# Kernel tuning notes

Hardware: AMD Instinct MI355X
Metric: run time of the kernel (lower is better)

Reference implementation:

```python
import jax, jax.numpy as jnp
import numpy as np

N_HEADS = 16
LOCAL_WINDOW = 256
GLOBAL_WINDOW = 1024


def _block_mha(x, in_proj_w, in_proj_b, out_proj_w, out_proj_b, window, n_heads):
    """Non-overlapping sliding-window MHA, matching torch nn.MultiheadAttention math.

    x: [B, S, D]; windows are independent -> fold them into the batch dim and do
    one batched attention (block-diagonal attention over the sequence).
    """
    B, S, D = x.shape
    nw = S // window
    hd = D // n_heads
    xw = x.reshape(B * nw, window, D)
    # combined QKV projection: in_proj_w is [3D, D], torch applies x @ W^T + b
    qkv = xw @ in_proj_w.T + in_proj_b  # [B*nw, W, 3D]
    q, k, v = jnp.split(qkv, 3, axis=-1)
    q = q.reshape(B * nw, window, n_heads, hd)
    k = k.reshape(B * nw, window, n_heads, hd)
    v = v.reshape(B * nw, window, n_heads, hd)
    scale = 1.0 / np.sqrt(hd).astype(np.float32)
    scores = jnp.einsum('bqhd,bkhd->bhqk', q, k) * scale
    attn = jax.nn.softmax(scores, axis=-1)
    out = jnp.einsum('bhqk,bkhd->bqhd', attn, v).reshape(B * nw, window, D)
    out = out @ out_proj_w.T + out_proj_b
    return out.reshape(B, S, D)


def setup_inputs() -> dict:
    key = jax.random.key(0)
    ks = jax.random.split(key, 8)
    B, S, D = 2, 4096, 1024
    w_scale = 1.0 / np.sqrt(D).astype(np.float32)
    return {
        'lqs': jax.random.normal(ks[0], (B, S, D), dtype=jnp.float32),
        'gqs': jax.random.normal(ks[1], (B, S, D), dtype=jnp.float32),
        'in_proj_w_l': jax.random.normal(ks[2], (3 * D, D), dtype=jnp.float32) * w_scale,
        'in_proj_b_l': jnp.zeros((3 * D,), dtype=jnp.float32),
        'out_proj_w_l': jax.random.normal(ks[3], (D, D), dtype=jnp.float32) * w_scale,
        'out_proj_b_l': jnp.zeros((D,), dtype=jnp.float32),
        'in_proj_w_g': jax.random.normal(ks[4], (3 * D, D), dtype=jnp.float32) * w_scale,
        'in_proj_b_g': jnp.zeros((3 * D,), dtype=jnp.float32),
        'out_proj_w_g': jax.random.normal(ks[5], (D, D), dtype=jnp.float32) * w_scale,
        'out_proj_b_g': jnp.zeros((D,), dtype=jnp.float32),
    }


def reference(lqs, gqs, in_proj_w_l, in_proj_b_l, out_proj_w_l, out_proj_b_l,
              in_proj_w_g, in_proj_b_g, out_proj_w_g, out_proj_b_g):
    local_out = _block_mha(lqs, in_proj_w_l, in_proj_b_l, out_proj_w_l, out_proj_b_l,
                           LOCAL_WINDOW, N_HEADS)
    global_out = _block_mha(gqs, in_proj_w_g, in_proj_b_g, out_proj_w_g, out_proj_b_g,
                            GLOBAL_WINDOW, N_HEADS)
    return (local_out, global_out)
```

## Files before the change

kernel.cpp:

```cpp
#include <hip/hip_runtime.h>
#include <stdint.h>

typedef __attribute__((ext_vector_type(8))) __bf16 bf16x8;
typedef __attribute__((ext_vector_type(4))) float f32x4;

__device__ __forceinline__ void async_ld16(const void* g, void* l) {
  __builtin_amdgcn_global_load_lds(
      (const __attribute__((address_space(1))) unsigned int*)g,
      (__attribute__((address_space(3))) unsigned int*)l, 16, 0, 0);
}

__device__ __forceinline__ unsigned short f2bf(float x) {
  union { float f; unsigned int u; } v; v.f = x;
  unsigned int r = v.u + 0x7FFFu + ((v.u >> 16) & 1u);
  return (unsigned short)(r >> 16);
}

__device__ __forceinline__ float exp2_fast(float x) {
  return __builtin_amdgcn_exp2f(x);
}

__device__ __forceinline__ unsigned int pack_bf2(float a, float b) {
  unsigned int ua = __builtin_bit_cast(unsigned int, a) + 0x8000u;
  unsigned int ub = __builtin_bit_cast(unsigned int, b) + 0x8000u;
  return __builtin_amdgcn_perm(ub, ua, 0x07060302u);
}

__global__ void cvt3(const float* __restrict__ x, unsigned short* __restrict__ xd,
                     const float* __restrict__ w1, unsigned short* __restrict__ w1d,
                     const float* __restrict__ w2, unsigned short* __restrict__ w2d) {
  int i = blockIdx.x * 256 + threadIdx.x;
  const float* s; unsigned short* d; int off;
  if (i < 2097152)      { s = x;  d = xd;  off = i; }
  else if (i < 2883584) { s = w1; d = w1d; off = i - 2097152; }
  else                  { s = w2; d = w2d; off = i - 2883584; }
  float4 v = ((const float4*)s)[off];
  ushort4 o;
  o.x = f2bf(v.x); o.y = f2bf(v.y); o.z = f2bf(v.z); o.w = f2bf(v.w);
  ((ushort4*)d)[off] = o;
}

__global__ __launch_bounds__(512, 2)
void gemm_bt(const unsigned short* __restrict__ A0, const unsigned short* __restrict__ A1,
             const unsigned short* __restrict__ B0, const unsigned short* __restrict__ B1,
             const float* __restrict__ bias0, const float* __restrict__ bias1,
             void* __restrict__ out0, void* __restrict__ out1,
             int N, int K, int f32out, int qlim, float qs) {
  __shared__ unsigned short As[2][2][256 * 32];
  __shared__ unsigned short Bs[2][2][256 * 32];
  int br = blockIdx.z;
  const unsigned short* A = br ? A1 : A0;
  const unsigned short* B = br ? B1 : B0;
  const float* bias = br ? bias1 : bias0;
  void* outp = br ? out1 : out0;

  int gx = gridDim.x, gy = gridDim.y;
  int nwg = gx * gy;
  int flat = blockIdx.y * gx + blockIdx.x;
  int cpx = nwg >> 3;
  int swb = (flat & 7) * cpx + (flat >> 3);
  int bxi = swb % gx, byi = swb / gx;

  int tid = threadIdx.x;
  int wave = tid >> 6, lane = tid & 63;
  int quad = lane >> 4, l16 = lane & 15;
  int wm = (wave >> 2) * 128;
  int wn = (wave & 3) * 64;
  size_t bm = (size_t)byi * 256, bn = (size_t)bxi * 256;

  f32x4 acc[8][4];
  f32x4 zero = {0.f, 0.f, 0.f, 0.f};
#pragma unroll
  for (int i = 0; i < 8; i++)
#pragma unroll
    for (int j = 0; j < 4; j++) acc[i][j] = zero;

  int swc = (quad ^ ((l16 >> 1) & 3)) * 16;
  const char* ArdB = (const char*)As + (wm + l16) * 64 + swc;
  const char* BrdB = (const char*)Bs + (wn + l16) * 64 + swc;

  int row0 = tid >> 2, c0 = (tid & 3) ^ ((row0 >> 1) & 3);
  int row1 = row0 + 128, c1 = (tid & 3) ^ ((row1 >> 1) & 3);
  const char* Ag0 = (const char*)(A + (bm + row0) * (size_t)K) + c0 * 16;
  const char* Ag1 = (const char*)(A + (bm + row1) * (size_t)K) + c1 * 16;
  const char* Bg0 = (const char*)(B + (bn + row0) * (size_t)K) + c0 * 16;
  const char* Bg1 = (const char*)(B + (bn + row1) * (size_t)K) + c1 * 16;
  char* ldsA = (char*)As + tid * 16;
  char* ldsB = (char*)Bs + tid * 16;

#define STAGE_A(po_, kh_, koff_) do {                    \
    char* d_ = ldsA + (po_) + (kh_) * 16384;             \
    async_ld16(Ag0 + (koff_), d_);                       \
    async_ld16(Ag1 + (koff_), d_ + 8192); } while (0)
#define STAGE_B(po_, kh_, koff_) do {                    \
    char* d_ = ldsB + (po_) + (kh_) * 16384;             \
    async_ld16(Bg0 + (koff_), d_);                       \
    async_ld16(Bg1 + (koff_), d_ + 8192); } while (0)
#define LDA_F(po_, kh_, mi_) (*(const bf16x8*)(ArdB + (po_) + (kh_) * 16384 + (mi_) * 1024))
#define LDB_F(po_, kh_, ni_) (*(const bf16x8*)(BrdB + (po_) + (kh_) * 16384 + (ni_) * 1024))
#define BAR() do { __builtin_amdgcn_s_barrier(); asm volatile("" ::: "memory"); } while (0)
#define MFMAQ(mb_) do {                                                                              \
    acc[(mb_)+0][0] = __builtin_amdgcn_mfma_f32_16x16x32_bf16(b0, a0, acc[(mb_)+0][0], 0, 0, 0);     \
    acc[(mb_)+1][0] = __builtin_amdgcn_mfma_f32_16x16x32_bf16(b0, a1, acc[(mb_)+1][0], 0, 0, 0);     \
    acc[(mb_)+2][0] = __builtin_amdgcn_mfma_f32_16x16x32_bf16(b0, a2, acc[(mb_)+2][0], 0, 0, 0);     \
    acc[(mb_)+3][0] = __builtin_amdgcn_mfma_f32_16x16x32_bf16(b0, a3, acc[(mb_)+3][0], 0, 0, 0);     \
    acc[(mb_)+0][1] = __builtin_amdgcn_mfma_f32_16x16x32_bf16(b1, a0, acc[(mb_)+0][1], 0, 0, 0);     \
    acc[(mb_)+1][1] = __builtin_amdgcn_mfma_f32_16x16x32_bf16(b1, a1, acc[(mb_)+1][1], 0, 0, 0);     \
    acc[(mb_)+2][1] = __builtin_amdgcn_mfma_f32_16x16x32_bf16(b1, a2, acc[(mb_)+2][1], 0, 0, 0);     \
    acc[(mb_)+3][1] = __builtin_amdgcn_mfma_f32_16x16x32_bf16(b1, a3, acc[(mb_)+3][1], 0, 0, 0);     \
    acc[(mb_)+0][2] = __builtin_amdgcn_mfma_f32_16x16x32_bf16(b2, a0, acc[(mb_)+0][2], 0, 0, 0);     \
    acc[(mb_)+1][2] = __builtin_amdgcn_mfma_f32_16x16x32_bf16(b2, a1, acc[(mb_)+1][2], 0, 0, 0);     \
    acc[(mb_)+2][2] = __builtin_amdgcn_mfma_f32_16x16x32_bf16(b2, a2, acc[(mb_)+2][2], 0, 0, 0);     \
    acc[(mb_)+3][2] = __builtin_amdgcn_mfma_f32_16x16x32_bf16(b2, a3, acc[(mb_)+3][2], 0, 0, 0);     \
    acc[(mb_)+0][3] = __builtin_amdgcn_mfma_f32_16x16x32_bf16(b3, a0, acc[(mb_)+0][3], 0, 0, 0);     \
    acc[(mb_)+1][3] = __builtin_amdgcn_mfma_f32_16x16x32_bf16(b3, a1, acc[(mb_)+1][3], 0, 0, 0);     \
    acc[(mb_)+2][3] = __builtin_amdgcn_mfma_f32_16x16x32_bf16(b3, a2, acc[(mb_)+2][3], 0, 0, 0);     \
    acc[(mb_)+3][3] = __builtin_amdgcn_mfma_f32_16x16x32_bf16(b3, a3, acc[(mb_)+3][3], 0, 0, 0);     \
  } while (0)

  const int NT = K >> 6;

  STAGE_A(0, 0, 0);       STAGE_B(0, 0, 0);
  STAGE_A(0, 1, 64);      STAGE_B(0, 1, 64);
  STAGE_A(32768, 0, 128); STAGE_B(32768, 0, 128);
  asm volatile("s_waitcnt vmcnt(4)" ::: "memory");
  BAR();

  for (int j = 0; j < NT; ++j) {
    int po = (j & 1) * 32768;
    int qo = po ^ 32768;
    int t1 = (j + 1 < NT) ? j + 1 : NT - 1;
    int t2 = (j + 2 < NT) ? j + 2 : NT - 1;
    int ko1 = t1 * 128 + 64;
    int ko2 = t2 * 128;
    bf16x8 a0, a1, a2, a3, b0, b1, b2, b3;

    b0 = LDB_F(po, 0, 0); b1 = LDB_F(po, 0, 1); b2 = LDB_F(po, 0, 2); b3 = LDB_F(po, 0, 3);
    a0 = LDA_F(po, 0, 0); a1 = LDA_F(po, 0, 1); a2 = LDA_F(po, 0, 2); a3 = LDA_F(po, 0, 3);
    STAGE_A(qo, 1, ko1);
    __builtin_amdgcn_s_setprio(1); MFMAQ(0); __builtin_amdgcn_s_setprio(0);
    BAR();
    a0 = LDA_F(po, 0, 4); a1 = LDA_F(po, 0, 5); a2 = LDA_F(po, 0, 6); a3 = LDA_F(po, 0, 7);
    STAGE_B(qo, 1, ko1);
    __builtin_amdgcn_s_setprio(1); MFMAQ(4); __builtin_amdgcn_s_setprio(0);
    asm volatile("s_waitcnt vmcnt(8)" ::: "memory");
    BAR();
    b0 = LDB_F(po, 1, 0); b1 = LDB_F(po, 1, 1); b2 = LDB_F(po, 1, 2); b3 = LDB_F(po, 1, 3);
    a0 = LDA_F(po, 1, 0); a1 = LDA_F(po, 1, 1); a2 = LDA_F(po, 1, 2); a3 = LDA_F(po, 1, 3);
    STAGE_A(po, 0, ko2);
    __builtin_amdgcn_s_setprio(1); MFMAQ(0); __builtin_amdgcn_s_setprio(0);
    BAR();
    a0 = LDA_F(po, 1, 4); a1 = LDA_F(po, 1, 5); a2 = LDA_F(po, 1, 6); a3 = LDA_F(po, 1, 7);
    STAGE_B(po, 0, ko2);
    __builtin_amdgcn_s_setprio(1); MFMAQ(4); __builtin_amdgcn_s_setprio(0);
    asm volatile("s_waitcnt vmcnt(8)" ::: "memory");
    BAR();
  }

#undef STAGE_A
#undef STAGE_B
#undef LDA_F
#undef LDB_F
#undef BAR
#undef MFMAQ

#pragma unroll
  for (int mi = 0; mi < 8; mi++) {
    size_t rowg = bm + wm + mi * 16 + l16;
#pragma unroll
    for (int ni = 0; ni < 4; ni++) {
      size_t col = bn + wn + ni * 16 + quad * 4;
      float s = ((int)col < qlim) ? qs : 1.0f;
      float4 bv = *(const float4*)&bias[col];
      f32x4 a = acc[mi][ni];
      if (f32out) {
        float4 o = {(a[0] + bv.x) * s, (a[1] + bv.y) * s,
                    (a[2] + bv.z) * s, (a[3] + bv.w) * s};
        *(float4*)&((float*)outp)[rowg * N + col] = o;
      } else {
        ushort4 o;
        o.x = f2bf((a[0] + bv.x) * s); o.y = f2bf((a[1] + bv.y) * s);
        o.z = f2bf((a[2] + bv.z) * s); o.w = f2bf((a[3] + bv.w) * s);
        *(ushort4*)&((unsigned short*)outp)[rowg * N + col] = o;
      }
    }
  }
}

__device__ __forceinline__ int kperm(int p) {
  return (p & 0xC3) | ((p & 0x0C) << 2) | ((p & 0x30) >> 2);
}
__global__ void transpose_v(const unsigned short* __restrict__ q0, unsigned short* __restrict__ v0, int W0,
                            const unsigned short* __restrict__ q1, unsigned short* __restrict__ v1, int W1,
                            int zsplit) {
  __shared__ unsigned short tile[64][33];
  int z = blockIdx.z;
  const unsigned short* qkv; unsigned short* vt; int W, wb, yy;
  if (z < zsplit) { qkv = q0; vt = v0; W = W0; wb = z; yy = blockIdx.y; }
  else { qkv = q1; vt = v1; W = W1; int t = z - zsplit; wb = t >> 2; yy = blockIdx.y + 4 * (t & 3); }
  int c0 = blockIdx.x * 32, w0 = yy * 64;
  const unsigned short* src = qkv + (size_t)wb * W * 3072 + 2048;
  for (int i = threadIdx.y; i < 64; i += 8)
    tile[i][threadIdx.x] = src[(size_t)(w0 + i) * 3072 + c0 + threadIdx.x];
  __syncthreads();
  unsigned short* dst = vt + (size_t)wb * 1024 * W;
  for (int i = threadIdx.y; i < 32; i += 8) {
    int p0 = threadIdx.x, p1 = threadIdx.x + 32;
    dst[(size_t)(c0 + i) * W + w0 + p0] = tile[kperm(p0)][i];
    dst[(size_t)(c0 + i) * W + w0 + p1] = tile[kperm(p1)][i];
  }
}

__global__ __launch_bounds__(256)
void attn_fused(const unsigned short* __restrict__ qkv0, const unsigned short* __restrict__ vt0,
                unsigned short* __restrict__ ao0, int W0, int nb0,
                const unsigned short* __restrict__ qkv1, const unsigned short* __restrict__ vt1,
                unsigned short* __restrict__ ao1, int W1) {
  __shared__ unsigned short Ks[64 * 64];
  __shared__ unsigned short Vs[64 * 64];
  __shared__ unsigned int   Ps[4][16 * 32];
  int bid = blockIdx.x;
  const unsigned short *qkv, *vtb0; unsigned short* ao; int W, rel;
  if (bid < nb0) { qkv = qkv0; vtb0 = vt0; ao = ao0; W = W0; rel = bid; }
  else           { qkv = qkv1; vtb0 = vt1; ao = ao1; W = W1; rel = bid - nb0; }
  int gx = W >> 7;
  int shift = (gx == 2) ? 1 : 3;
  int bx = rel & (gx - 1);
  int wbh = rel >> shift;
  int wb = wbh >> 4, h = wbh & 15;

  int tid = threadIdx.x;
  int wave = tid >> 6, lane = tid & 63;
  int quad = lane >> 4, l16 = lane & 15;
  int swz = l16 & 7;
  int q0w = bx * 128 + wave * 32;

  const unsigned short* qb = qkv + (size_t)wb * W * 3072 + h * 64;
  const unsigned short* kb = qb + 1024;
  const unsigned short* vtb = vtb0 + (size_t)wbh * 64 * W;

  bf16x8 qf[2][2];
  for (int cb = 0; cb < 2; cb++)
    for (int ch = 0; ch < 2; ch++)
      qf[cb][ch] = *(const bf16x8*)(qb + (size_t)(q0w + cb * 16 + l16) * 3072 +
                                    ch * 32 + quad * 8);

  f32x4 zero = {0.f, 0.f, 0.f, 0.f};
  f32x4 O[2][4];
  for (int cb = 0; cb < 2; cb++)
    for (int g = 0; g < 4; g++) O[cb][g] = zero;
  float l_i[2] = {0.f, 0.f};

  for (int k0 = 0; k0 < W; k0 += 64) {
    __syncthreads();
    for (int j = 0; j < 2; j++) {
      int c = j * 256 + tid;
      int row = c >> 3, sl = c & 7, ss = sl ^ (row & 7);
      async_ld16(kb + (size_t)(k0 + row) * 3072 + ss * 8, (char*)Ks + c * 16);
      async_ld16(vtb + (size_t)row * W + k0 + ss * 8,     (char*)Vs + c * 16);
    }
    __syncthreads();

    bf16x8 ak[4][2], vf[4][2];
#pragma unroll
    for (int i = 0; i < 4; i++)
#pragma unroll
      for (int ch = 0; ch < 2; ch++) {
        int sl = (ch * 4 + quad) ^ swz;
        ak[i][ch] = *(const bf16x8*)&Ks[(i * 16 + l16) * 64 + sl * 8];
        vf[i][ch] = *(const bf16x8*)&Vs[(i * 16 + l16) * 64 + sl * 8];
      }

    for (int cb = 0; cb < 2; cb++) {
      unsigned int pk[8];
      float sm = 0.f;
#pragma unroll
      for (int sub = 0; sub < 4; sub++) {
        f32x4 z = zero;
        z = __builtin_amdgcn_mfma_f32_16x16x32_bf16(ak[sub][0], qf[cb][0], z, 0, 0, 0);
        z = __builtin_amdgcn_mfma_f32_16x16x32_bf16(ak[sub][1], qf[cb][1], z, 0, 0, 0);
        float p0 = exp2_fast(z[0]), p1 = exp2_fast(z[1]);
        float p2 = exp2_fast(z[2]), p3 = exp2_fast(z[3]);
        sm += (p0 + p1) + (p2 + p3);
        pk[((sub & 1) * 2) + (sub >> 1) * 4]     = pack_bf2(p0, p1);
        pk[((sub & 1) * 2) + (sub >> 1) * 4 + 1] = pack_bf2(p2, p3);
      }
      sm += __shfl_xor(sm, 16);
      sm += __shfl_xor(sm, 32);
      l_i[cb] += sm;

      unsigned int* pw = &Ps[wave][0];
      uint4 u0 = {pk[0], pk[1], pk[2], pk[3]};
      uint4 u1 = {pk[4], pk[5], pk[6], pk[7]};
      *(uint4*)&pw[l16 * 32 + ((2 * quad) ^ swz) * 4]     = u0;
      *(uint4*)&pw[l16 * 32 + ((2 * quad + 1) ^ swz) * 4] = u1;

      bf16x8 pf[2];
#pragma unroll
      for (int ch = 0; ch < 2; ch++) {
        uint4 u = *(const uint4*)&pw[l16 * 32 + ((ch * 4 + quad) ^ swz) * 4];
        pf[ch] = __builtin_bit_cast(bf16x8, u);
      }
#pragma unroll
      for (int g = 0; g < 4; g++) {
        O[cb][g] = __builtin_amdgcn_mfma_f32_16x16x32_bf16(pf[0], vf[g][0], O[cb][g], 0, 0, 0);
        O[cb][g] = __builtin_amdgcn_mfma_f32_16x16x32_bf16(pf[1], vf[g][1], O[cb][g], 0, 0, 0);
      }
    }
  }

  for (int cb = 0; cb < 2; cb++) {
    float inv = 1.0f / l_i[cb];
    float ivr[4];
    for (int r = 0; r < 4; r++) ivr[r] = __shfl(inv, quad * 4 + r);
    for (int r = 0; r < 4; r++) {
      size_t rowg = (size_t)wb * W + q0w + cb * 16 + quad * 4 + r;
      for (int g = 0; g < 4; g++)
        ao[rowg * 1024 + h * 64 + g * 16 + l16] = f2bf(O[cb][g][r] * ivr[r]);
    }
  }
}

extern "C" void kernel_launch(void* const* d_in, const int* in_sizes, int n_in,
                              void* d_out, int out_size, void* d_ws, size_t ws_size,
                              hipStream_t stream) {
  const int D = 1024, TD = 3072, M = 8192;
  const float QS = 0.125f * 1.44269504089f;
  const size_t PER = 46137344;
  bool comb = ws_size >= (size_t)2 * PER * 2;

  unsigned short* Xb[2]; unsigned short* Wb[2]; unsigned short* Ob[2];
  unsigned short* qkv[2]; unsigned short* vt[2];
  for (int b = 0; b < 2; b++) {
    unsigned short* base = (unsigned short*)d_ws + (comb ? b * PER : 0);
    Xb[b]  = base;
    Wb[b]  = Xb[b] + 8388608;
    Ob[b]  = Wb[b] + 3145728;
    qkv[b] = Ob[b] + 1048576;
    vt[b]  = qkv[b] + 25165824;
  }
  float* outp = (float*)d_out;
  const float* x[2]   = {(const float*)d_in[0], (const float*)d_in[1]};
  const float* ipw[2] = {(const float*)d_in[2], (const float*)d_in[6]};
  const float* ipb[2] = {(const float*)d_in[3], (const float*)d_in[7]};
  const float* opw[2] = {(const float*)d_in[4], (const float*)d_in[8]};
  const float* opb[2] = {(const float*)d_in[5], (const float*)d_in[9]};
  const int Wd[2] = {256, 1024};

  if (comb) {
    for (int b = 0; b < 2; b++)
      cvt3<<<12288, 256, 0, stream>>>(x[b], Xb[b], ipw[b], Wb[b], opw[b], Ob[b]);
    gemm_bt<<<dim3(TD / 256, M / 256, 2), 512, 0, stream>>>(
        Xb[0], Xb[1], Wb[0], Wb[1], ipb[0], ipb[1], qkv[0], qkv[1],
        TD, D, 0, D, QS);
    transpose_v<<<dim3(32, 4, 64), dim3(32, 8), 0, stream>>>(
        qkv[0], vt[0], 256, qkv[1], vt[1], 1024, 32);
    attn_fused<<<2048, 256, 0, stream>>>(
        qkv[0], vt[0], Xb[0], 256, 1024, qkv[1], vt[1], Xb[1], 1024);
    gemm_bt<<<dim3(D / 256, M / 256, 2), 512, 0, stream>>>(
        Xb[0], Xb[1], Ob[0], Ob[1], opb[0], opb[1], outp, outp + 8388608,
        D, D, 1, 0, 1.0f);
  } else {
    for (int b = 0; b < 2; b++) {
      int W = Wd[b], nwb = M / W;
      cvt3<<<12288, 256, 0, stream>>>(x[b], Xb[b], ipw[b], Wb[b], opw[b], Ob[b]);
      gemm_bt<<<dim3(TD / 256, M / 256, 1), 512, 0, stream>>>(
          Xb[b], Xb[b], Wb[b], Wb[b], ipb[b], ipb[b], qkv[b], qkv[b],
          TD, D, 0, D, QS);
      if (b == 0)
        transpose_v<<<dim3(32, 4, 32), dim3(32, 8), 0, stream>>>(
            qkv[b], vt[b], W, qkv[b], vt[b], W, 32);
      else
        transpose_v<<<dim3(32, 4, 32), dim3(32, 8), 0, stream>>>(
            qkv[b], vt[b], W, qkv[b], vt[b], W, 0);
      int nb = (W >> 7) * nwb * 16;
      attn_fused<<<nb, 256, 0, stream>>>(
          qkv[b], vt[b], Xb[b], W, nb, qkv[b], vt[b], Xb[b], W);
      gemm_bt<<<dim3(D / 256, M / 256, 1), 512, 0, stream>>>(
          Xb[b], Xb[b], Ob[b], Ob[b], opb[b], opb[b],
          outp + (size_t)b * 8388608, outp + (size_t)b * 8388608,
          D, D, 1, 0, 1.0f);
    }
  }
}
```

Measured before the change: 414.6 us.

## Double-buffer MFMA fragment registers to overlap LDS reads with matrix math

Restructures the GEMM main loop so LDS fragment loads for the next MFMA quarter are issued into a separate register set before the current quarter's MFMAs run, with a prologue preloading the first fragments. The async global-to-LDS staging order and vmcnt waits are reshuffled accordingly, and one extra stage is issued in the prologue. The aim is to hide LDS read latency behind MFMA work. The cost is more VGPRs for the doubled fragment registers, which may reduce occupancy, plus a more delicate barrier and waitcnt schedule.

```diff
diff --git a/kernel.cpp b/kernel.cpp
--- a/kernel.cpp
+++ b/kernel.cpp
@@ -99,61 +99,74 @@
 #define LDA_F(po_, kh_, mi_) (*(const bf16x8*)(ArdB + (po_) + (kh_) * 16384 + (mi_) * 1024))
 #define LDB_F(po_, kh_, ni_) (*(const bf16x8*)(BrdB + (po_) + (kh_) * 16384 + (ni_) * 1024))
 #define BAR() do { __builtin_amdgcn_s_barrier(); asm volatile("" ::: "memory"); } while (0)
-#define MFMAQ(mb_) do {                                                                              \
-    acc[(mb_)+0][0] = __builtin_amdgcn_mfma_f32_16x16x32_bf16(b0, a0, acc[(mb_)+0][0], 0, 0, 0);     \
-    acc[(mb_)+1][0] = __builtin_amdgcn_mfma_f32_16x16x32_bf16(b0, a1, acc[(mb_)+1][0], 0, 0, 0);     \
-    acc[(mb_)+2][0] = __builtin_amdgcn_mfma_f32_16x16x32_bf16(b0, a2, acc[(mb_)+2][0], 0, 0, 0);     \
-    acc[(mb_)+3][0] = __builtin_amdgcn_mfma_f32_16x16x32_bf16(b0, a3, acc[(mb_)+3][0], 0, 0, 0);     \
-    acc[(mb_)+0][1] = __builtin_amdgcn_mfma_f32_16x16x32_bf16(b1, a0, acc[(mb_)+0][1], 0, 0, 0);     \
-    acc[(mb_)+1][1] = __builtin_amdgcn_mfma_f32_16x16x32_bf16(b1, a1, acc[(mb_)+1][1], 0, 0, 0);     \
-    acc[(mb_)+2][1] = __builtin_amdgcn_mfma_f32_16x16x32_bf16(b1, a2, acc[(mb_)+2][1], 0, 0, 0);     \
-    acc[(mb_)+3][1] = __builtin_amdgcn_mfma_f32_16x16x32_bf16(b1, a3, acc[(mb_)+3][1], 0, 0, 0);     \
-    acc[(mb_)+0][2] = __builtin_amdgcn_mfma_f32_16x16x32_bf16(b2, a0, acc[(mb_)+0][2], 0, 0, 0);     \
-    acc[(mb_)+1][2] = __builtin_amdgcn_mfma_f32_16x16x32_bf16(b2, a1, acc[(mb_)+1][2], 0, 0, 0);     \
-    acc[(mb_)+2][2] = __builtin_amdgcn_mfma_f32_16x16x32_bf16(b2, a2, acc[(mb_)+2][2], 0, 0, 0);     \
-    acc[(mb_)+3][2] = __builtin_amdgcn_mfma_f32_16x16x32_bf16(b2, a3, acc[(mb_)+3][2], 0, 0, 0);     \
-    acc[(mb_)+0][3] = __builtin_amdgcn_mfma_f32_16x16x32_bf16(b3, a0, acc[(mb_)+0][3], 0, 0, 0);     \
-    acc[(mb_)+1][3] = __builtin_amdgcn_mfma_f32_16x16x32_bf16(b3, a1, acc[(mb_)+1][3], 0, 0, 0);     \
-    acc[(mb_)+2][3] = __builtin_amdgcn_mfma_f32_16x16x32_bf16(b3, a2, acc[(mb_)+2][3], 0, 0, 0);     \
-    acc[(mb_)+3][3] = __builtin_amdgcn_mfma_f32_16x16x32_bf16(b3, a3, acc[(mb_)+3][3], 0, 0, 0);     \
+#define MFMAQ(mb_, B0_, B1_, B2_, B3_, A0_, A1_, A2_, A3_) do {                                        \
+    acc[(mb_)+0][0] = __builtin_amdgcn_mfma_f32_16x16x32_bf16(B0_, A0_, acc[(mb_)+0][0], 0, 0, 0);     \
+    acc[(mb_)+1][0] = __builtin_amdgcn_mfma_f32_16x16x32_bf16(B0_, A1_, acc[(mb_)+1][0], 0, 0, 0);     \
+    acc[(mb_)+2][0] = __builtin_amdgcn_mfma_f32_16x16x32_bf16(B0_, A2_, acc[(mb_)+2][0], 0, 0, 0);     \
+    acc[(mb_)+3][0] = __builtin_amdgcn_mfma_f32_16x16x32_bf16(B0_, A3_, acc[(mb_)+3][0], 0, 0, 0);     \
+    acc[(mb_)+0][1] = __builtin_amdgcn_mfma_f32_16x16x32_bf16(B1_, A0_, acc[(mb_)+0][1], 0, 0, 0);     \
+    acc[(mb_)+1][1] = __builtin_amdgcn_mfma_f32_16x16x32_bf16(B1_, A1_, acc[(mb_)+1][1], 0, 0, 0);     \
+    acc[(mb_)+2][1] = __builtin_amdgcn_mfma_f32_16x16x32_bf16(B1_, A2_, acc[(mb_)+2][1], 0, 0, 0);     \
+    acc[(mb_)+3][1] = __builtin_amdgcn_mfma_f32_16x16x32_bf16(B1_, A3_, acc[(mb_)+3][1], 0, 0, 0);     \
+    acc[(mb_)+0][2] = __builtin_amdgcn_mfma_f32_16x16x32_bf16(B2_, A0_, acc[(mb_)+0][2], 0, 0, 0);     \
+    acc[(mb_)+1][2] = __builtin_amdgcn_mfma_f32_16x16x32_bf16(B2_, A1_, acc[(mb_)+1][2], 0, 0, 0);     \
+    acc[(mb_)+2][2] = __builtin_amdgcn_mfma_f32_16x16x32_bf16(B2_, A2_, acc[(mb_)+2][2], 0, 0, 0);     \
+    acc[(mb_)+3][2] = __builtin_amdgcn_mfma_f32_16x16x32_bf16(B2_, A3_, acc[(mb_)+3][2], 0, 0, 0);     \
+    acc[(mb_)+0][3] = __builtin_amdgcn_mfma_f32_16x16x32_bf16(B3_, A0_, acc[(mb_)+0][3], 0, 0, 0);     \
+    acc[(mb_)+1][3] = __builtin_amdgcn_mfma_f32_16x16x32_bf16(B3_, A1_, acc[(mb_)+1][3], 0, 0, 0);     \
+    acc[(mb_)+2][3] = __builtin_amdgcn_mfma_f32_16x16x32_bf16(B3_, A2_, acc[(mb_)+2][3], 0, 0, 0);     \
+    acc[(mb_)+3][3] = __builtin_amdgcn_mfma_f32_16x16x32_bf16(B3_, A3_, acc[(mb_)+3][3], 0, 0, 0);     \
   } while (0)
 
   const int NT = K >> 6;
+
+  bf16x8 bX0, bX1, bX2, bX3;
+  bf16x8 bY0, bY1, bY2, bY3;
+  bf16x8 aP0, aP1, aP2, aP3;
+  bf16x8 aQ0, aQ1, aQ2, aQ3;
 
   STAGE_A(0, 0, 0);       STAGE_B(0, 0, 0);
   STAGE_A(0, 1, 64);      STAGE_B(0, 1, 64);
   STAGE_A(32768, 0, 128); STAGE_B(32768, 0, 128);
-  asm volatile("s_waitcnt vmcnt(4)" ::: "memory");
+  STAGE_A(32768, 1, 192);
+  asm volatile("s_waitcnt vmcnt(10)" ::: "memory");
   BAR();
+  bX0 = LDB_F(0, 0, 0); bX1 = LDB_F(0, 0, 1); bX2 = LDB_F(0, 0, 2); bX3 = LDB_F(0, 0, 3);
+  aP0 = LDA_F(0, 0, 0); aP1 = LDA_F(0, 0, 1); aP2 = LDA_F(0, 0, 2); aP3 = LDA_F(0, 0, 3);
 
   for (int j = 0; j < NT; ++j) {
     int po = (j & 1) * 32768;
     int qo = po ^ 32768;
-    int t1 = (j + 1 < NT) ? j + 1 : NT - 1;
-    int t2 = (j + 2 < NT) ? j + 2 : NT - 1;
-    int ko1 = t1 * 128 + 64;
-    int ko2 = t2 * 128;
-    bf16x8 a0, a1, a2, a3, b0, b1, b2, b3;
-
-    b0 = LDB_F(po, 0, 0); b1 = LDB_F(po, 0, 1); b2 = LDB_F(po, 0, 2); b3 = LDB_F(po, 0, 3);
-    a0 = LDA_F(po, 0, 0); a1 = LDA_F(po, 0, 1); a2 = LDA_F(po, 0, 2); a3 = LDA_F(po, 0, 3);
-    STAGE_A(qo, 1, ko1);
-    __builtin_amdgcn_s_setprio(1); MFMAQ(0); __builtin_amdgcn_s_setprio(0);
-    BAR();
-    a0 = LDA_F(po, 0, 4); a1 = LDA_F(po, 0, 5); a2 = LDA_F(po, 0, 6); a3 = LDA_F(po, 0, 7);
-    STAGE_B(qo, 1, ko1);
-    __builtin_amdgcn_s_setprio(1); MFMAQ(4); __builtin_amdgcn_s_setprio(0);
+    int ko1 = ((j + 1 < NT) ? j + 1 : NT - 1) * 128;
+    int ko2 = ((j + 2 < NT) ? j + 2 : NT - 1) * 128;
+
+    aQ0 = LDA_F(po, 0, 4); aQ1 = LDA_F(po, 0, 5); aQ2 = LDA_F(po, 0, 6); aQ3 = LDA_F(po, 0, 7);
+    STAGE_B(qo, 1, ko1 + 64);
+    __builtin_amdgcn_s_setprio(1);
+    MFMAQ(0, bX0, bX1, bX2, bX3, aP0, aP1, aP2, aP3);
+    __builtin_amdgcn_s_setprio(0);
     asm volatile("s_waitcnt vmcnt(8)" ::: "memory");
     BAR();
-    b0 = LDB_F(po, 1, 0); b1 = LDB_F(po, 1, 1); b2 = LDB_F(po, 1, 2); b3 = LDB_F(po, 1, 3);
-    a0 = LDA_F(po, 1, 0); a1 = LDA_F(po, 1, 1); a2 = LDA_F(po, 1, 2); a3 = LDA_F(po, 1, 3);
+    bY0 = LDB_F(po, 1, 0); bY1 = LDB_F(po, 1, 1); bY2 = LDB_F(po, 1, 2); bY3 = LDB_F(po, 1, 3);
+    aP0 = LDA_F(po, 1, 0); aP1 = LDA_F(po, 1, 1); aP2 = LDA_F(po, 1, 2); aP3 = LDA_F(po, 1, 3);
     STAGE_A(po, 0, ko2);
-    __builtin_amdgcn_s_setprio(1); MFMAQ(0); __builtin_amdgcn_s_setprio(0);
+    __builtin_amdgcn_s_setprio(1);
+    MFMAQ(4, bX0, bX1, bX2, bX3, aQ0, aQ1, aQ2, aQ3);
+    __builtin_amdgcn_s_setprio(0);
     BAR();
-    a0 = LDA_F(po, 1, 4); a1 = LDA_F(po, 1, 5); a2 = LDA_F(po, 1, 6); a3 = LDA_F(po, 1, 7);
+    aQ0 = LDA_F(po, 1, 4); aQ1 = LDA_F(po, 1, 5); aQ2 = LDA_F(po, 1, 6); aQ3 = LDA_F(po, 1, 7);
     STAGE_B(po, 0, ko2);
-    __builtin_amdgcn_s_setprio(1); MFMAQ(4); __builtin_amdgcn_s_setprio(0);
+    __builtin_amdgcn_s_setprio(1);
+    MFMAQ(0, bY0, bY1, bY2, bY3, aP0, aP1, aP2, aP3);
+    __builtin_amdgcn_s_setprio(0);
     asm volatile("s_waitcnt vmcnt(8)" ::: "memory");
+    BAR();
+    bX0 = LDB_F(qo, 0, 0); bX1 = LDB_F(qo, 0, 1); bX2 = LDB_F(qo, 0, 2); bX3 = LDB_F(qo, 0, 3);
+    aP0 = LDA_F(qo, 0, 0); aP1 = LDA_F(qo, 0, 1); aP2 = LDA_F(qo, 0, 2); aP3 = LDA_F(qo, 0, 3);
+    STAGE_A(po, 1, ko2 + 64);
+    __builtin_amdgcn_s_setprio(1);
+    MFMAQ(4, bY0, bY1, bY2, bY3, aQ0, aQ1, aQ2, aQ3);
+    __builtin_amdgcn_s_setprio(0);
     BAR();
   }
 
```

New measurement: 413.5 us. No clear change (-0.3%).

## Double-buffer K/V tiles in attention and use raw asm barriers in GEMM

Applied to the files above, without the earlier changes.

The attention kernel now keeps two LDS buffers for K and V. It prefetches the next 64-key tile asynchronously while computing on the current one, and the second __syncthreads per iteration is gone. The aim is to hide global-to-LDS load latency behind the MFMA and softmax work. The GEMM barrier macro is replaced by an inline-asm s_barrier, which may change how the compiler places waits around it. The cost is double the K/V LDS footprint, which could lower occupancy. Correctness now depends on the top-of-loop barrier also draining the outstanding async loads.

```diff
diff --git a/kernel.cpp b/kernel.cpp
--- a/kernel.cpp
+++ b/kernel.cpp
@@ -98,7 +98,7 @@
     async_ld16(Bg1 + (koff_), d_ + 8192); } while (0)
 #define LDA_F(po_, kh_, mi_) (*(const bf16x8*)(ArdB + (po_) + (kh_) * 16384 + (mi_) * 1024))
 #define LDB_F(po_, kh_, ni_) (*(const bf16x8*)(BrdB + (po_) + (kh_) * 16384 + (ni_) * 1024))
-#define BAR() do { __builtin_amdgcn_s_barrier(); asm volatile("" ::: "memory"); } while (0)
+#define BARA() asm volatile("s_barrier" ::: "memory")
 #define MFMAQ(mb_) do {                                                                              \
     acc[(mb_)+0][0] = __builtin_amdgcn_mfma_f32_16x16x32_bf16(b0, a0, acc[(mb_)+0][0], 0, 0, 0);     \
     acc[(mb_)+1][0] = __builtin_amdgcn_mfma_f32_16x16x32_bf16(b0, a1, acc[(mb_)+1][0], 0, 0, 0);     \
@@ -124,7 +124,7 @@
   STAGE_A(0, 1, 64);      STAGE_B(0, 1, 64);
   STAGE_A(32768, 0, 128); STAGE_B(32768, 0, 128);
   asm volatile("s_waitcnt vmcnt(4)" ::: "memory");
-  BAR();
+  BARA();
 
   for (int j = 0; j < NT; ++j) {
     int po = (j & 1) * 32768;
@@ -139,29 +139,29 @@
     a0 = LDA_F(po, 0, 0); a1 = LDA_F(po, 0, 1); a2 = LDA_F(po, 0, 2); a3 = LDA_F(po, 0, 3);
     STAGE_A(qo, 1, ko1);
     __builtin_amdgcn_s_setprio(1); MFMAQ(0); __builtin_amdgcn_s_setprio(0);
-    BAR();
+    BARA();
     a0 = LDA_F(po, 0, 4); a1 = LDA_F(po, 0, 5); a2 = LDA_F(po, 0, 6); a3 = LDA_F(po, 0, 7);
     STAGE_B(qo, 1, ko1);
     __builtin_amdgcn_s_setprio(1); MFMAQ(4); __builtin_amdgcn_s_setprio(0);
     asm volatile("s_waitcnt vmcnt(8)" ::: "memory");
-    BAR();
+    BARA();
     b0 = LDB_F(po, 1, 0); b1 = LDB_F(po, 1, 1); b2 = LDB_F(po, 1, 2); b3 = LDB_F(po, 1, 3);
     a0 = LDA_F(po, 1, 0); a1 = LDA_F(po, 1, 1); a2 = LDA_F(po, 1, 2); a3 = LDA_F(po, 1, 3);
     STAGE_A(po, 0, ko2);
     __builtin_amdgcn_s_setprio(1); MFMAQ(0); __builtin_amdgcn_s_setprio(0);
-    BAR();
+    BARA();
     a0 = LDA_F(po, 1, 4); a1 = LDA_F(po, 1, 5); a2 = LDA_F(po, 1, 6); a3 = LDA_F(po, 1, 7);
     STAGE_B(po, 0, ko2);
     __builtin_amdgcn_s_setprio(1); MFMAQ(4); __builtin_amdgcn_s_setprio(0);
     asm volatile("s_waitcnt vmcnt(8)" ::: "memory");
-    BAR();
+    BARA();
   }
 
 #undef STAGE_A
 #undef STAGE_B
 #undef LDA_F
 #undef LDB_F
-#undef BAR
+#undef BARA
 #undef MFMAQ
 
 #pragma unroll
@@ -216,8 +216,8 @@
                 unsigned short* __restrict__ ao0, int W0, int nb0,
                 const unsigned short* __restrict__ qkv1, const unsigned short* __restrict__ vt1,
                 unsigned short* __restrict__ ao1, int W1) {
-  __shared__ unsigned short Ks[64 * 64];
-  __shared__ unsigned short Vs[64 * 64];
+  __shared__ unsigned short Ks[2][64 * 64];
+  __shared__ unsigned short Vs[2][64 * 64];
   __shared__ unsigned int   Ps[4][16 * 32];
   int bid = blockIdx.x;
   const unsigned short *qkv, *vtb0; unsigned short* ao; int W, rel;
@@ -251,15 +251,29 @@
     for (int g = 0; g < 4; g++) O[cb][g] = zero;
   float l_i[2] = {0.f, 0.f};
 
-  for (int k0 = 0; k0 < W; k0 += 64) {
+  {
+    int c0s = tid, c1s = 256 + tid;
+    int r0 = c0s >> 3, s0 = (c0s & 7) ^ (r0 & 7);
+    int r1 = c1s >> 3, s1 = (c1s & 7) ^ (r1 & 7);
+    async_ld16(kb + (size_t)r0 * 3072 + s0 * 8, (char*)&Ks[0][0] + c0s * 16);
+    async_ld16(vtb + (size_t)r0 * W + s0 * 8,   (char*)&Vs[0][0] + c0s * 16);
+    async_ld16(kb + (size_t)r1 * 3072 + s1 * 8, (char*)&Ks[0][0] + c1s * 16);
+    async_ld16(vtb + (size_t)r1 * W + s1 * 8,   (char*)&Vs[0][0] + c1s * 16);
+  }
+
+  int it = 0;
+  for (int k0 = 0; k0 < W; k0 += 64, ++it) {
+    int cur = it & 1;
     __syncthreads();
-    for (int j = 0; j < 2; j++) {
-      int c = j * 256 + tid;
-      int row = c >> 3, sl = c & 7, ss = sl ^ (row & 7);
-      async_ld16(kb + (size_t)(k0 + row) * 3072 + ss * 8, (char*)Ks + c * 16);
-      async_ld16(vtb + (size_t)row * W + k0 + ss * 8,     (char*)Vs + c * 16);
-    }
-    __syncthreads();
+    if (k0 + 64 < W) {
+      int nxt = cur ^ 1, kk = k0 + 64;
+      for (int j = 0; j < 2; j++) {
+        int c = j * 256 + tid;
+        int row = c >> 3, sl = c & 7, ss = sl ^ (row & 7);
+        async_ld16(kb + (size_t)(kk + row) * 3072 + ss * 8, (char*)&Ks[nxt][0] + c * 16);
+        async_ld16(vtb + (size_t)row * W + kk + ss * 8,     (char*)&Vs[nxt][0] + c * 16);
+      }
+    }
 
     bf16x8 ak[4][2], vf[4][2];
 #pragma unroll
@@ -267,8 +281,8 @@
 #pragma unroll
       for (int ch = 0; ch < 2; ch++) {
         int sl = (ch * 4 + quad) ^ swz;
-        ak[i][ch] = *(const bf16x8*)&Ks[(i * 16 + l16) * 64 + sl * 8];
-        vf[i][ch] = *(const bf16x8*)&Vs[(i * 16 + l16) * 64 + sl * 8];
+        ak[i][ch] = *(const bf16x8*)&Ks[cur][(i * 16 + l16) * 64 + sl * 8];
+        vf[i][ch] = *(const bf16x8*)&Vs[cur][(i * 16 + l16) * 64 + sl * 8];
       }
 
     for (int cb = 0; cb < 2; cb++) {
```

Result: no change. 415.1 us (+0.1%).
